# Kernel optimization log

Hardware: AMD Instinct MI355X
Metric: run time of the kernel (lower is better)

## Reference

```python
import jax, jax.numpy as jnp
import numpy as np

BS, EP = 32, 32
N_AGENTS, N_ATOM, EMBED = 8, 51, 32
STATE_DIM, HYP = 128, 64
V_MIN, V_MAX = -10.0, 10.0


def proj(support, probs, v_min, v_max, n_atom):
    # C51 categorical projection of (support, probs) onto the fixed atom grid
    # linspace(v_min, v_max, n_atom). support/probs: [..., M] -> [..., n_atom]
    support, probs = jnp.broadcast_arrays(support, probs)
    delta = (v_max - v_min) / (n_atom - 1)
    b = (jnp.clip(support, v_min, v_max) - v_min) / delta
    l = jnp.floor(b)
    u = jnp.ceil(b)
    eq = (u == l).astype(probs.dtype)  # support exactly on an atom -> all mass to l
    ml = probs * (u - b + eq)
    mu = probs * (b - l)
    shp = probs.shape
    n = int(np.prod(shp[:-1]))
    m = shp[-1]
    rows = jnp.arange(n)[:, None]
    out = jnp.zeros((n, n_atom), probs.dtype)
    out = out.at[rows, l.astype(jnp.int32).reshape(n, m)].add(ml.reshape(n, m))
    out = out.at[rows, u.astype(jnp.int32).reshape(n, m)].add(mu.reshape(n, m))
    return out.reshape(shp[:-1] + (n_atom,))


def bconv(p, q):
    # Full 1D convolution of per-row categorical pmfs (sum of two random vars).
    # p: [N, L], q: [N, M] -> [N, L+M-1], via grouped conv (one group per row).
    N, L = p.shape
    M = q.shape[-1]
    out = jax.lax.conv_general_dilated(
        p[None], jnp.flip(q, -1)[:, None, :],
        window_strides=(1,), padding=[(M - 1, M - 1)],
        feature_group_count=N, dimension_numbers=('NCW', 'OIW', 'NCW'))
    return out[0]


def mlp2(x, w1, b1, w2, b2):
    return jax.nn.relu(x @ w1.T + b1) @ w2.T + b2


def setup_inputs():
    key = jax.random.key(0)
    ks = jax.random.split(key, 20)
    def p(k, shape, s=0.05):
        return jax.random.normal(k, shape, dtype=jnp.float32) * s
    aq = jax.random.uniform(ks[0], (BS, EP, N_AGENTS, N_ATOM), dtype=jnp.float32)
    aq = aq / jnp.sum(aq, -1, keepdims=True)  # valid categorical distributions
    return {
        'agent_qs_distri': aq,
        'states': p(ks[1], (BS, EP, STATE_DIM), 1.0),
        'hw1_w1': p(ks[2], (HYP, STATE_DIM)), 'hw1_b1': p(ks[3], (HYP,)),
        'hw1_w2': p(ks[4], (EMBED * N_AGENTS, HYP)), 'hw1_b2': p(ks[5], (EMBED * N_AGENTS,)),
        'hb1_w': p(ks[6], (EMBED, STATE_DIM)), 'hb1_b': p(ks[7], (EMBED,)),
        'hwf_w1': p(ks[8], (HYP, STATE_DIM)), 'hwf_b1': p(ks[9], (HYP,)),
        'hwf_w2': p(ks[10], (EMBED, HYP)), 'hwf_b2': p(ks[11], (EMBED,)),
        'v_w1': p(ks[12], (EMBED, STATE_DIM)), 'v_b1': p(ks[13], (EMBED,)),
        'v_w2': p(ks[14], (1, EMBED)), 'v_b2': p(ks[15], (1,)),
    }


def reference(agent_qs_distri, states, hw1_w1, hw1_b1, hw1_w2, hw1_b2,
              hb1_w, hb1_b, hwf_w1, hwf_b1, hwf_w2, hwf_b2,
              v_w1, v_b1, v_w2, v_b2):
    bs, ep, n_agents, n_atom = agent_qs_distri.shape
    s = states.reshape(-1, STATE_DIM)
    atoms = jnp.linspace(V_MIN, V_MAX, n_atom).astype(jnp.float32)  # [A]

    w1 = jnp.abs(mlp2(s, hw1_w1, hw1_b1, hw1_w2, hw1_b2)).reshape(bs, ep, EMBED, n_agents)
    b1 = (s @ hb1_w.T + hb1_b).reshape(bs, ep, EMBED)

    # stage 1: scale each agent's support by w1[..., k, i], project back onto atoms
    sup1 = atoms * w1[..., None]                                       # [bs,ep,E,Na,A]
    aw = proj(sup1, agent_qs_distri[:, :, None], V_MIN, V_MAX, n_atom)  # [bs,ep,E,Na,A]
    awf = aw.reshape(-1, n_agents, n_atom)                              # [bs*ep*E,Na,A]
    q = awf[:, 0]
    for i in range(1, n_agents):
        q = bconv(q, awf[:, i])                                         # [.., Na*A-Na+1]
    L1 = n_agents * n_atom - n_agents + 1
    sup = jnp.linspace(n_agents * V_MIN, n_agents * V_MAX, L1).astype(jnp.float32)
    sup = jax.nn.elu(sup + b1[..., None])                               # [bs,ep,E,L1]
    x = proj(sup, q.reshape(bs, ep, EMBED, L1), V_MIN, V_MAX, n_atom)   # [bs,ep,E,A]

    # stage 2: hyper_w_final scaling, convolve across embed dim, add V(s)
    wf = jnp.abs(mlp2(s, hwf_w1, hwf_b1, hwf_w2, hwf_b2)).reshape(bs, ep, EMBED)
    xw = proj(atoms * wf[..., None], x, V_MIN, V_MAX, n_atom)           # [bs,ep,E,A]
    xwf = xw.reshape(-1, EMBED, n_atom)
    q = xwf[:, 0]
    for i in range(1, EMBED):
        q = bconv(q, xwf[:, i])                                         # [bs*ep, E*A-E+1]
    L2 = EMBED * n_atom - EMBED + 1
    v = mlp2(s, v_w1, v_b1, v_w2, v_b2).reshape(bs, ep, 1)
    sup2 = jnp.linspace(EMBED * V_MIN, EMBED * V_MAX, L2).astype(jnp.float32) + v
    return proj(sup2, q.reshape(bs, ep, L2), V_MIN, V_MAX, n_atom)      # [bs,ep,A]
```

## Files before the change

kernel.cpp:

```cpp
#include <hip/hip_runtime.h>
#include <hip/hip_bf16.h>
#include <math.h>

typedef unsigned short u16;

#define WAVE_SYNC() asm volatile("s_waitcnt lgkmcnt(0)" ::: "memory")

__device__ __forceinline__ float bf2f(u16 u) {
  union { unsigned int i; float f; } c;
  c.i = ((unsigned int)u) << 16;
  return c.f;
}
__device__ __forceinline__ float bflo(unsigned int u) {
  union { unsigned int i; float f; } c; c.i = u << 16; return c.f;
}
__device__ __forceinline__ float bfhi(unsigned int u) {
  union { unsigned int i; float f; } c; c.i = u & 0xffff0000u; return c.f;
}
__device__ __forceinline__ u16 f2bf(float f) {
  union { float f; unsigned int i; } c;
  c.f = f;
  unsigned int x = c.i;
  unsigned int r = (x + 0x7fffu + ((x >> 16) & 1u)) >> 16;
  return (u16)r;
}

__device__ __forceinline__ void proj_bounds(float wv, int& ML, int& MH) {
  float smin = (-10.0f + 0.4f * 0.0f)  * wv;
  float smax = (-10.0f + 0.4f * 50.0f) * wv;
  float bmin = (fminf(fmaxf(smin, -10.0f), 10.0f) + 10.0f) / 0.4f;
  float bmax = (fminf(fmaxf(smax, -10.0f), 10.0f) + 10.0f) / 0.4f;
  ML = (int)floorf(bmin);
  MH = (int)ceilf(bmax);
}

template<typename SUPP>
__device__ __forceinline__ void proj_scan(float* __restrict__ g1,
                                          float* __restrict__ g2,
                                          int span, int lane, SUPP supp)
{
  if (lane < 52) g1[lane] = 0.f;
  if (lane < 53) g2[lane] = 0.f;
  float cml = 0.f, cmu = 0.f;
  int ck = -1;
  for (int base = 0; base < span; base += 64) {
    int t = base + lane;
    bool act = (t < span);
    int tc = act ? t : (span - 1);
    float sup, p;
    supp(tc, act, sup, p);
    float c  = fminf(fmaxf(sup, -10.0f), 10.0f);
    float b  = (c + 10.0f) / 0.4f;
    float l  = floorf(b);
    float u  = ceilf(b);
    float eq = (u == l) ? 1.0f : 0.0f;
    float ml = p * (u - b + eq);
    float mu = p * (b - l);
    int   li = (int)l;
    bool last = (base + 64 >= span);
    if (lane == 0 && ck >= 0) {
      if (ck == li) { ml += cml; mu += cmu; }
      else          { g1[ck] = cml; g2[ck + 1] = cmu; }
    }
#pragma unroll
    for (int d = 1; d < 64; d <<= 1) {
      int   lo = __shfl_up(li, d);
      float a1 = __shfl_up(ml, d);
      float a2 = __shfl_up(mu, d);
      bool same = (lane >= d) && (lo == li);
      ml += same ? a1 : 0.f;
      mu += same ? a2 : 0.f;
    }
    int ln = __shfl_down(li, 1);
    bool runend = (lane == 63) ? last : (ln != li);
    if (runend) { g1[li] = ml; g2[li + 1] = mu; }
    if (!last) {
      cml = __shfl(ml, 63);
      cmu = __shfl(mu, 63);
      ck  = __shfl(li, 63);
    }
  }
}

__device__ __forceinline__ void conv_pad2(const float* __restrict__ q,
                                          float* __restrict__ qn,
                                          const float* __restrict__ kvs,
                                          int ML, int W, int T,
                                          int LQ, int HQ, int tid, int nthr)
{
  const int Lout = LQ + ML, Hout = HQ + ML + T;
  for (int J = Lout + tid; J <= Hout; J += nthr) {
    const float* qp = q + (J - ML);
    float acc = 0.f;
    for (int c = 0; c < W; c += 4) {
      float4 k4 = *(const float4*)(kvs + c);
      acc = fmaf(k4.x, qp[-c],     acc);
      acc = fmaf(k4.y, qp[-c - 1], acc);
      acc = fmaf(k4.z, qp[-c - 2], acc);
      acc = fmaf(k4.w, qp[-c - 3], acc);
    }
    qn[J] = acc;
  }
}

template<int BF>
__device__ __forceinline__ float ldt(const void* p, int i) {
  if (BF) return bf2f(((const u16*)p)[i]);
  return ((const float*)p)[i];
}

template<int BF>
__device__ __forceinline__ float dot128_t(const void* w, int row, const float* s) {
  float acc = 0.f;
  if (BF) {
    const uint4* p = (const uint4*)((const u16*)w + row * 128);
#pragma unroll
    for (int i = 0; i < 16; ++i) {
      uint4 v = p[i];
      int b = i * 8;
      acc = fmaf(bflo(v.x), s[b + 0], acc); acc = fmaf(bfhi(v.x), s[b + 1], acc);
      acc = fmaf(bflo(v.y), s[b + 2], acc); acc = fmaf(bfhi(v.y), s[b + 3], acc);
      acc = fmaf(bflo(v.z), s[b + 4], acc); acc = fmaf(bfhi(v.z), s[b + 5], acc);
      acc = fmaf(bflo(v.w), s[b + 6], acc); acc = fmaf(bfhi(v.w), s[b + 7], acc);
    }
  } else {
    const float4* p = (const float4*)((const float*)w + row * 128);
#pragma unroll
    for (int i = 0; i < 32; ++i) {
      float4 v = p[i];
      int b = i * 4;
      acc = fmaf(v.x, s[b + 0], acc); acc = fmaf(v.y, s[b + 1], acc);
      acc = fmaf(v.z, s[b + 2], acc); acc = fmaf(v.w, s[b + 3], acc);
    }
  }
  return acc;
}

template<int BF>
__device__ __forceinline__ float dot64_t(const void* w, int row, const float* h) {
  float acc = 0.f;
  if (BF) {
    const uint4* p = (const uint4*)((const u16*)w + row * 64);
#pragma unroll
    for (int i = 0; i < 8; ++i) {
      uint4 v = p[i];
      int b = i * 8;
      acc = fmaf(bflo(v.x), h[b + 0], acc); acc = fmaf(bfhi(v.x), h[b + 1], acc);
      acc = fmaf(bflo(v.y), h[b + 2], acc); acc = fmaf(bfhi(v.y), h[b + 3], acc);
      acc = fmaf(bflo(v.z), h[b + 4], acc); acc = fmaf(bfhi(v.z), h[b + 5], acc);
      acc = fmaf(bflo(v.w), h[b + 6], acc); acc = fmaf(bfhi(v.w), h[b + 7], acc);
    }
  } else {
    const float4* p = (const float4*)((const float*)w + row * 64);
#pragma unroll
    for (int i = 0; i < 16; ++i) {
      float4 v = p[i];
      int b = i * 4;
      acc = fmaf(v.x, h[b + 0], acc); acc = fmaf(v.y, h[b + 1], acc);
      acc = fmaf(v.z, h[b + 2], acc); acc = fmaf(v.w, h[b + 3], acc);
    }
  }
  return acc;
}

template<int BF>
__device__ __forceinline__ void mlp_body(
    const void* states,
    const void* hw1_w1, const void* hw1_b1, const void* hw1_w2, const void* hw1_b2,
    const void* hb1_w,  const void* hb1_b,
    const void* hwf_w1, const void* hwf_b1, const void* hwf_w2, const void* hwf_b2,
    const void* v_w1,   const void* v_b1,   const void* v_w2,   const void* v_b2,
    float* w1_ws, float* b1_ws, float* wf_ws, float* v_ws,
    int n, int tid, float* s, float* h1, float* hf, float* vh)
{
  s[tid]      = ldt<BF>(states, n * 128 + tid);
  s[tid + 64] = ldt<BF>(states, n * 128 + 64 + tid);
  __syncthreads();

  h1[tid] = fmaxf(dot128_t<BF>(hw1_w1, tid, s) + ldt<BF>(hw1_b1, tid), 0.f);
  hf[tid] = fmaxf(dot128_t<BF>(hwf_w1, tid, s) + ldt<BF>(hwf_b1, tid), 0.f);
  if (tid < 32) {
    vh[tid] = fmaxf(dot128_t<BF>(v_w1, tid, s) + ldt<BF>(v_b1, tid), 0.f);
    b1_ws[n * 32 + tid] = dot128_t<BF>(hb1_w, tid, s) + ldt<BF>(hb1_b, tid);
  }
  __syncthreads();

#pragma unroll
  for (int k = 0; k < 4; ++k) {
    int o = tid + 64 * k;
    w1_ws[n * 256 + o] = fabsf(dot64_t<BF>(hw1_w2, o, h1) + ldt<BF>(hw1_b2, o));
  }
  if (tid < 32)
    wf_ws[n * 32 + tid] = fabsf(dot64_t<BF>(hwf_w2, tid, hf) + ldt<BF>(hwf_b2, tid));
  if (tid == 0) {
    float acc = ldt<BF>(v_b2, 0);
    for (int e = 0; e < 32; ++e) acc = fmaf(ldt<BF>(v_w2, e), vh[e], acc);
    v_ws[n] = acc;
  }
}

__global__ __launch_bounds__(64) void k_mlp(
    const void* __restrict__ states,
    const void* __restrict__ hw1_w1, const void* __restrict__ hw1_b1,
    const void* __restrict__ hw1_w2, const void* __restrict__ hw1_b2,
    const void* __restrict__ hb1_w,  const void* __restrict__ hb1_b,
    const void* __restrict__ hwf_w1, const void* __restrict__ hwf_b1,
    const void* __restrict__ hwf_w2, const void* __restrict__ hwf_b2,
    const void* __restrict__ v_w1,   const void* __restrict__ v_b1,
    const void* __restrict__ v_w2,   const void* __restrict__ v_b2,
    float* __restrict__ w1_ws, float* __restrict__ b1_ws,
    float* __restrict__ wf_ws, float* __restrict__ v_ws,
    int* __restrict__ flag)
{
  __shared__ float s[128];
  __shared__ float h1[64];
  __shared__ float hf[64];
  __shared__ float vh[32];
  const int n = blockIdx.x;
  const int tid = threadIdx.x;

  const u16* sr = (const u16*)states;
  unsigned int e0 = (sr[tid] >> 7) & 0xFF;
  unsigned int e1 = (sr[tid + 64] >> 7) & 0xFF;
  unsigned long long bl0 = __ballot(e0 >= 97 && e0 <= 141);
  unsigned long long bl1 = __ballot(e1 >= 97 && e1 <= 141);
  int bf = (__popcll(bl0) + __popcll(bl1) >= 104) ? 1 : 0;
  if (tid == 0) *flag = bf;

  if (bf)
    mlp_body<1>(states, hw1_w1, hw1_b1, hw1_w2, hw1_b2, hb1_w, hb1_b,
                hwf_w1, hwf_b1, hwf_w2, hwf_b2, v_w1, v_b1, v_w2, v_b2,
                w1_ws, b1_ws, wf_ws, v_ws, n, tid, s, h1, hf, vh);
  else
    mlp_body<0>(states, hw1_w1, hw1_b1, hw1_w2, hw1_b2, hb1_w, hb1_b,
                hwf_w1, hwf_b1, hwf_w2, hwf_b2, v_w1, v_b1, v_w2, v_b2,
                w1_ws, b1_ws, wf_ws, v_ws, n, tid, s, h1, hf, vh);
}

__global__ __launch_bounds__(128) void k_perembed(
    const void* __restrict__ aq,
    const float* __restrict__ w1_ws, const float* __restrict__ b1_ws,
    const float* __restrict__ wf_ws, float* __restrict__ xw_ws,
    const int* __restrict__ flag)
{
  __shared__ __align__(16) float Ab[2][520];
  __shared__ __align__(16) float Bb[2][520];
  __shared__ __align__(16) float kv_all[2][8][16];
  __shared__ __align__(16) float kvo[2][56];
  __shared__ float p_lds[2][8][52];
  __shared__ float gAb[2][53];
  __shared__ float gBb[2][54];

  const int w    = threadIdx.x >> 6;
  const int lane = threadIdx.x & 63;
  const int task = blockIdx.x * 2 + w;
  const int n = task >> 5;
  const int e = task & 31;
  const int bf = *flag;

  float* A   = Ab[w];
  float* B   = Bb[w];
  float* gA  = gAb[w];
  float* gB  = gBb[w];
  float (*pl)[52] = p_lds[w];

  if (bf) {
    const u16* p = (const u16*)aq + n * 408 + lane;
    if (lane < 51) {
#pragma unroll
      for (int a = 0; a < 8; ++a) pl[a][lane] = bf2f(p[a * 51]);
    }
  } else {
    const float* p = (const float*)aq + n * 408 + lane;
    if (lane < 51) {
#pragma unroll
      for (int a = 0; a < 8; ++a) pl[a][lane] = p[a * 51];
    }
  }
  float wreg = (lane < 8) ? w1_ws[n * 256 + e * 8 + lane] : 0.f;
  float b1v  = b1_ws[n * 32 + e];
  float wfv  = wf_ws[n * 32 + e];

  int mlA = 0, mhA = 0;
  if (lane < 8) proj_bounds(wreg, mlA, mhA);
  unsigned long long wide = __ballot((lane < 8) && (mhA - mlA > 15));
  WAVE_SYNC();

  int LQ, HQ;
  float* q = A;
  float* qn = B;

  if (wide == 0ull) {
#pragma unroll
    for (int r = 0; r < 2; ++r) {
      int a  = 4 * r + (lane >> 4);
      int jj = lane & 15;
      float wv = __shfl(wreg, a);
      int ML = __shfl(mlA, a);
      int MH = __shfl(mhA, a);
      int T = MH - ML;
      int j = ML + jj;
      float ej = 0.4f * (float)j - 10.0f;
      float invw = 2.5f / wv;
      int tL = (jj == 0) ? 0  : (int)floorf((ej - 0.4f) * invw + 25.f) - 1;
      int tH = (jj >= T) ? 50 : (int)ceilf ((ej + 0.4f) * invw + 25.f) + 1;
      tL = tL < 0 ? 0 : tL;
      tH = tH > 50 ? 50 : tH;
      if (jj > T) { tL = 0; tH = -1; }
      float acc = 0.f;
      float tf = (float)tL;
      const float* pb = pl[a];
      for (int t = tL; t <= tH; ++t) {
        float p = pb[t];
        float sup = (-10.0f + 0.4f * tf) * wv;
        float c = fminf(fmaxf(sup, -10.0f), 10.0f);
        float d = (c - ej) * 2.5f;
        float wgt = fmaxf(0.f, 1.f - fabsf(d));
        acc = fmaf(p, wgt, acc);
        tf += 1.0f;
      }
      kv_all[w][a][jj] = (jj <= T) ? acc : 0.f;
    }
    WAVE_SYNC();

    int ML0 = __shfl(mlA, 0), MH0 = __shfl(mhA, 0);
    if (lane <= MH0 - ML0) A[64 + ML0 + lane] = kv_all[w][0][lane];
    WAVE_SYNC();
    LQ = 64 + ML0; HQ = 64 + MH0;

#pragma unroll
    for (int a = 1; a < 8; ++a) {
      int ML = __shfl(mlA, a), MH = __shfl(mhA, a);
      int T = MH - ML;
      int W = (T + 4) & ~3;
      if (lane < W - 1) q[LQ - 1 - lane] = 0.f;
      if (lane < T)     q[HQ + 1 + lane] = 0.f;
      WAVE_SYNC();
      conv_pad2(q, qn, &kv_all[w][a][0], ML, W, T, LQ, HQ, lane, 64);
      WAVE_SYNC();
      LQ += ML; HQ += MH;
      float* t_ = q; q = qn; qn = t_;
    }
  } else {
    float* kvs = kvo[w];
    float wv0 = __shfl(wreg, 0);
    int ML0 = __shfl(mlA, 0), MH0 = __shfl(mhA, 0);
    proj_scan(gA, gB, 51, lane, [&](int t, bool act, float& sup, float& p) {
      sup = (-10.0f + 0.4f * (float)t) * wv0;
      float pv = pl[0][t];
      p = act ? pv : 0.f;
    });
    if (lane <= MH0 - ML0)
      A[64 + ML0 + lane] = gA[ML0 + lane] + gB[ML0 + lane];
    WAVE_SYNC();
    LQ = 64 + ML0; HQ = 64 + MH0;

    for (int a = 1; a < 8; ++a) {
      float wv = __shfl(wreg, a);
      int ML = __shfl(mlA, a), MH = __shfl(mhA, a);
      int T = MH - ML;
      int W = (T + 4) & ~3;
      proj_scan(gA, gB, 51, lane, [&](int t, bool act, float& sup, float& p) {
        sup = (-10.0f + 0.4f * (float)t) * wv;
        float pv = pl[a][t];
        p = act ? pv : 0.f;
      });
      if (lane < W)     kvs[lane] = (lane <= T) ? (gA[ML + lane] + gB[ML + lane]) : 0.f;
      if (lane < W - 1) q[LQ - 1 - lane] = 0.f;
      if (lane < T)     q[HQ + 1 + lane] = 0.f;
      WAVE_SYNC();
      conv_pad2(q, qn, kvs, ML, W, T, LQ, HQ, lane, 64);
      WAVE_SYNC();
      LQ += ML; HQ += MH;
      float* t_ = q; q = qn; qn = t_;
    }
  }

  {
    int span = HQ - LQ + 1;
    int LQl = LQ;
    const float* qf = q;
    proj_scan(gA, gB, span, lane, [&](int t, bool act, float& sup, float& p) {
      int tg = (LQl - 64) + t;
      float raw = (-80.0f + 0.4f * (float)tg) + b1v;
      sup = (raw > 0.f) ? raw : expm1f(raw);
      p = act ? qf[LQl + t] : 0.f;
    });
  }
  WAVE_SYNC();

  float x2v = (lane < 51) ? (gA[lane] + gB[lane]) : 0.f;
  WAVE_SYNC();
  int MLf, MHf;
  proj_bounds(wfv, MLf, MHf);
  proj_scan(gA, gB, 51, lane, [&](int t, bool act, float& sup, float& p) {
    sup = (-10.0f + 0.4f * (float)t) * wfv;
    p = act ? x2v : 0.f;
  });
  WAVE_SYNC();
  if (lane <= MHf - MLf)
    xw_ws[task * 51 + MLf + lane] = gA[MLf + lane] + gB[MLf + lane];
}

__global__ __launch_bounds__(256) void k_final(
    const float* __restrict__ xw_ws, const float* __restrict__ wf_ws,
    const float* __restrict__ v_ws,
    void* __restrict__ out, const int* __restrict__ flag)
{
  __shared__ __align__(16) float bufA[4608];
  __shared__ __align__(16) float bufB[4608];
  __shared__ int meta_s[63];
  __shared__ int meta_l[63];
  __shared__ int meta_ml[32];
  __shared__ int meta_g[6];
  __shared__ int meta_mltot;
  __shared__ float gA[53], gB[54];

  const int n    = blockIdx.x;
  const int tid  = threadIdx.x;
  const int lane = tid & 63;
  const int bf   = *flag;

  float wfreg = (lane < 32) ? wf_ws[n * 32 + lane] : 0.f;
  float vv    = v_ws[n];

  for (int i = tid; i < 4608; i += 256) { bufA[i] = 0.f; bufB[i] = 0.f; }

  if (tid < 64) {
    int ml, mh;
    proj_bounds(wfreg, ml, mh);
    if (lane < 32) meta_ml[lane] = ml;
    int msum = ml;
#pragma unroll
    for (int d = 1; d < 32; d <<= 1) msum += __shfl_xor(msum, d);
    if (lane == 0) meta_mltot = msum;

    int curlen = mh - ml + 1;
    int base = 0, Ncur = 32;
#pragma unroll
    for (int c = 0; c <= 5; ++c) {
      int lm = (lane < Ncur) ? curlen : 0;
#pragma unroll
      for (int d = 1; d < 32; d <<= 1) {
        int o = __shfl_xor(lm, d);
        lm = (o > lm) ? o : lm;
      }
      int G = (lm + 11) & ~3;
      int sp = ((curlen + 3) & ~3) + G;
      int inc = (lane < Ncur) ? sp : 0;
      int v0 = inc;
#pragma unroll
      for (int d = 1; d < 32; d <<= 1) {
        int u = __shfl_up(inc, d);
        if (lane >= d && lane < 32) inc += u;
      }
      if (lane < Ncur) {
        meta_s[base + lane] = 832 + (inc - v0);
        meta_l[base + lane] = curlen;
      }
      if (lane == 0) meta_g[c] = G;
      if (c < 5) {
        int l0 = __shfl(curlen, 2 * lane);
        int l1 = __shfl(curlen, 2 * lane + 1);
        curlen = l0 + l1 - 1;
        base += Ncur;
        Ncur >>= 1;
      }
    }
  }
  __syncthreads();

  {
    int g = tid >> 3, i = tid & 7;
    int s = meta_s[g], l = meta_l[g], ml = meta_ml[g];
    const float* row = xw_ws + (n * 32 + g) * 51 + ml;
    for (int i0 = i; i0 < l; i0 += 8) bufA[s + i0] = row[i0];
  }
  __syncthreads();

#pragma unroll
  for (int c = 1; c <= 5; ++c) {
    const float* bin = (c & 1) ? bufA : bufB;
    float*       bout = (c & 1) ? bufB : bufA;
    const int Nout = 32 >> c;
    const int lg = 3 + c;
    const int gs = 1 << lg;
    const int k  = tid >> lg;
    const int st = tid & (gs - 1);
    const int bc = 64 - (64 >> c);
    const int bp = 64 - (64 >> (c - 1));
    const int i0 = bp + 2 * k;
    const int sA = meta_s[i0];
    const int sB = meta_s[i0 + 1];
    const int lB = meta_l[i0 + 1];
    const int sO = meta_s[bc + k];
    const int lO = meta_l[bc + k];
    const int W  = (lB + 3) & ~3;

    for (int j = st * 2; j < lO; j += gs * 2) {
      const float* Ap = bin + sA + j + 1;
      float a0 = 0.f, a1 = 0.f;
      for (int m = 0; m < W; m += 4) {
        float4 k4 = *(const float4*)(bin + sB + m);
        float v0 = Ap[-m], v1 = Ap[-m - 1], v2 = Ap[-m - 2];
        float v3 = Ap[-m - 3], v4 = Ap[-m - 4];
        a0 = fmaf(k4.x, v1, fmaf(k4.y, v2, fmaf(k4.z, v3, fmaf(k4.w, v4, a0))));
        a1 = fmaf(k4.x, v0, fmaf(k4.y, v1, fmaf(k4.z, v2, fmaf(k4.w, v3, a1))));
      }
      bout[sO + j] = a0;
      if (j + 1 < lO) bout[sO + j + 1] = a1;
    }

    if (c >= 2 && c <= 4) {
      int G = meta_g[c];
      for (int p = tid; p < G; p += 256) bout[832 - G + p] = 0.f;
      for (int k2 = 0; k2 < Nout; ++k2) {
        int ss = meta_s[bc + k2] + meta_l[bc + k2];
        int ee = (k2 + 1 < Nout) ? meta_s[bc + k2 + 1]
                                 : ss + G + 3;
        for (int p = ss + tid; p < ee; p += 256) bout[p] = 0.f;
      }
    }
    __syncthreads();
  }

  if (tid < 64) {
    int s5 = meta_s[62], l5 = meta_l[62], mlt = meta_mltot;
    const float* qf = bufB + s5;
    proj_scan(gA, gB, l5, lane, [&](int t, bool act, float& sup, float& p) {
      int tg = mlt + t;
      sup = (-320.0f + 0.4f * (float)tg) + vv;
      p = act ? qf[t] : 0.f;
    });
    WAVE_SYNC();
    if (lane < 51) {
      float o = gA[lane] + gB[lane];
      if (bf) ((u16*)out)[n * 51 + lane] = f2bf(o);
      else    ((float*)out)[n * 51 + lane] = o;
    }
  }
}

extern "C" void kernel_launch(void* const* d_in, const int* in_sizes, int n_in,
                              void* d_out, int out_size, void* d_ws, size_t ws_size,
                              hipStream_t stream)
{
  float* ws    = (float*)d_ws;
  float* w1_ws = ws;
  float* b1_ws = w1_ws + 1024 * 256;
  float* wf_ws = b1_ws + 1024 * 32;
  float* v_ws  = wf_ws + 1024 * 32;
  float* xw_ws = v_ws  + 1024;
  int*   flag  = (int*)(xw_ws + 1024 * 32 * 51);

  k_mlp<<<1024, 64, 0, stream>>>(d_in[1],
      d_in[2], d_in[3], d_in[4], d_in[5], d_in[6], d_in[7],
      d_in[8], d_in[9], d_in[10], d_in[11], d_in[12], d_in[13],
      d_in[14], d_in[15],
      w1_ws, b1_ws, wf_ws, v_ws, flag);

  k_perembed<<<16384, 128, 0, stream>>>(d_in[0], w1_ws, b1_ws, wf_ws, xw_ws, flag);

  k_final<<<1024, 256, 0, stream>>>(xw_ws, wf_ws, v_ws, d_out, flag);
}
```

Baseline: 248.7 us.

## Trim zero-tail kernel spans and merge per-agent convolution barriers

In the narrow path of the per-embed kernel, each projected agent kernel is trimmed to its nonzero span using a wave ballot, so later convolutions run over shorter windows. The zero padding for the next step is written right after the current convolution, which removes one wave sync per agent. The ping-pong buffers are pre-zeroed once with float4 stores, and the final kernel's buffer clearing now uses float4 stores and runs the bounds computation in every wave instead of a tid<64 guard. This depends on the pre-zeroed buffers staying correct for the high-side padding that was dropped, and misaligned or shifted kernel windows could break correctness.

```diff
diff --git a/kernel.cpp b/kernel.cpp
--- a/kernel.cpp
+++ b/kernel.cpp
@@ -245,9 +245,10 @@
 {
   __shared__ __align__(16) float Ab[2][520];
   __shared__ __align__(16) float Bb[2][520];
-  __shared__ __align__(16) float kv_all[2][8][16];
+  __shared__ __align__(16) float kv_all[2][8][20];
   __shared__ __align__(16) float kvo[2][56];
   __shared__ float p_lds[2][8][52];
+  __shared__ int   tml[2][8], tmh[2][8];
   __shared__ float gAb[2][53];
   __shared__ float gBb[2][54];
 
@@ -263,6 +264,13 @@
   float* gA  = gAb[w];
   float* gB  = gBb[w];
   float (*pl)[52] = p_lds[w];
+
+  {
+    float4 z = make_float4(0.f, 0.f, 0.f, 0.f);
+    float4* a4 = (float4*)A;
+    float4* b4 = (float4*)B;
+    for (int i = lane; i < 130; i += 64) { a4[i] = z; b4[i] = z; }
+  }
 
   if (bf) {
     const u16* p = (const u16*)aq + n * 408 + lane;
@@ -300,45 +308,61 @@
       int MH = __shfl(mhA, a);
       int T = MH - ML;
       int j = ML + jj;
-      float ej = 0.4f * (float)j - 10.0f;
+      float ej  = 0.4f * (float)j - 10.0f;
+      float e25 = ej * 2.5f;
       float invw = 2.5f / wv;
       int tL = (jj == 0) ? 0  : (int)floorf((ej - 0.4f) * invw + 25.f) - 1;
       int tH = (jj >= T) ? 50 : (int)ceilf ((ej + 0.4f) * invw + 25.f) + 1;
       tL = tL < 0 ? 0 : tL;
       tH = tH > 50 ? 50 : tH;
       if (jj > T) { tL = 0; tH = -1; }
+      float step = 0.4f * wv;
+      float sup  = fmaf((float)tL, step, -10.0f * wv);
       float acc = 0.f;
-      float tf = (float)tL;
       const float* pb = pl[a];
       for (int t = tL; t <= tH; ++t) {
-        float p = pb[t];
-        float sup = (-10.0f + 0.4f * tf) * wv;
-        float c = fminf(fmaxf(sup, -10.0f), 10.0f);
-        float d = (c - ej) * 2.5f;
-        float wgt = fmaxf(0.f, 1.f - fabsf(d));
-        acc = fmaf(p, wgt, acc);
-        tf += 1.0f;
-      }
-      kv_all[w][a][jj] = (jj <= T) ? acc : 0.f;
+        float c   = fminf(fmaxf(sup, -10.0f), 10.0f);
+        float d   = fmaf(c, 2.5f, -e25);
+        float wgt = fmaxf(0.f, 1.0f - fabsf(d));
+        acc = fmaf(pb[t], wgt, acc);
+        sup += step;
+      }
+      unsigned long long nz = __ballot(acc != 0.f);
+      unsigned int field = (unsigned int)((nz >> (16 * (lane >> 4))) & 0xFFFFull);
+      int o_lo = 0, o_hi = T;
+      if (field) { o_lo = (__ffs(field) - 1) & ~3; o_hi = 31 - __clz(field); }
+      if (jj == 0) { tml[w][a] = ML + o_lo; tmh[w][a] = ML + o_hi; }
+      kv_all[w][a][jj] = acc;
+      if (jj < 4) kv_all[w][a][16 + jj] = 0.f;
     }
     WAVE_SYNC();
 
-    int ML0 = __shfl(mlA, 0), MH0 = __shfl(mhA, 0);
-    if (lane <= MH0 - ML0) A[64 + ML0 + lane] = kv_all[w][0][lane];
+    int ML0o = __shfl(mlA, 0);
+    int t0l = tml[w][0], t0h = tmh[w][0];
+    if (lane <= t0h - t0l) A[64 + t0l + lane] = kv_all[w][0][(t0l - ML0o) + lane];
+    LQ = 64 + t0l; HQ = 64 + t0h;
+
+    {
+      int ML1 = tml[w][1], MH1 = tmh[w][1];
+      int W1 = ((MH1 - ML1) + 4) & ~3;
+      if (lane < W1 - 1) A[LQ - 1 - lane] = 0.f;
+    }
     WAVE_SYNC();
-    LQ = 64 + ML0; HQ = 64 + MH0;
 
 #pragma unroll
     for (int a = 1; a < 8; ++a) {
-      int ML = __shfl(mlA, a), MH = __shfl(mhA, a);
+      int MLo = __shfl(mlA, a);
+      int ML = tml[w][a], MH = tmh[w][a];
       int T = MH - ML;
       int W = (T + 4) & ~3;
-      if (lane < W - 1) q[LQ - 1 - lane] = 0.f;
-      if (lane < T)     q[HQ + 1 + lane] = 0.f;
+      conv_pad2(q, qn, &kv_all[w][a][ML - MLo], ML, W, T, LQ, HQ, lane, 64);
+      LQ += ML; HQ += MH;
+      if (a < 7) {
+        int MLn = tml[w][a + 1], MHn = tmh[w][a + 1];
+        int Wn = ((MHn - MLn) + 4) & ~3;
+        if (lane < Wn - 1) qn[LQ - 1 - lane] = 0.f;
+      }
       WAVE_SYNC();
-      conv_pad2(q, qn, &kv_all[w][a][0], ML, W, T, LQ, HQ, lane, 64);
-      WAVE_SYNC();
-      LQ += ML; HQ += MH;
       float* t_ = q; q = qn; qn = t_;
     }
   } else {
@@ -367,7 +391,6 @@
       });
       if (lane < W)     kvs[lane] = (lane <= T) ? (gA[ML + lane] + gB[ML + lane]) : 0.f;
       if (lane < W - 1) q[LQ - 1 - lane] = 0.f;
-      if (lane < T)     q[HQ + 1 + lane] = 0.f;
       WAVE_SYNC();
       conv_pad2(q, qn, kvs, ML, W, T, LQ, HQ, lane, 64);
       WAVE_SYNC();
@@ -424,9 +447,14 @@
   float wfreg = (lane < 32) ? wf_ws[n * 32 + lane] : 0.f;
   float vv    = v_ws[n];
 
-  for (int i = tid; i < 4608; i += 256) { bufA[i] = 0.f; bufB[i] = 0.f; }
-
-  if (tid < 64) {
+  {
+    float4 z = make_float4(0.f, 0.f, 0.f, 0.f);
+    float4* a4 = (float4*)bufA;
+    float4* b4 = (float4*)bufB;
+    for (int i = tid; i < 1152; i += 256) { a4[i] = z; b4[i] = z; }
+  }
+
+  {
     int ml, mh;
     proj_bounds(wfreg, ml, mh);
     if (lane < 32) meta_ml[lane] = ml;
```

New measurement: 250.1 us. About the same (+0.6%).

## Fuse final embed convolution into per-embed kernel via last-arriving wave

Applied to the files above, without the earlier changes.

Each per-embed wave atomically bumps a per-sample counter. The last of the 32 waves then runs the 32-way convolution and final projection in its own LDS arena, writes the output and sets a done flag, while samples whose support is too wide fall back to k_final, which now exits early when the flag is set. This removes the k_final tail work and the extra round-trip through memory for most samples, at the cost of serialising a 31-step convolution on a single wave and enlarging LDS per block. It also strength-reduces the support computation in the first-stage projection loop and vectorises the zero fill in k_final.

```diff
diff --git a/kernel.cpp b/kernel.cpp
--- a/kernel.cpp
+++ b/kernel.cpp
@@ -210,7 +210,7 @@
     const void* __restrict__ v_w2,   const void* __restrict__ v_b2,
     float* __restrict__ w1_ws, float* __restrict__ b1_ws,
     float* __restrict__ wf_ws, float* __restrict__ v_ws,
-    int* __restrict__ flag)
+    int* __restrict__ flag, int* __restrict__ cnt, int* __restrict__ done)
 {
   __shared__ float s[128];
   __shared__ float h1[64];
@@ -225,7 +225,7 @@
   unsigned long long bl0 = __ballot(e0 >= 97 && e0 <= 141);
   unsigned long long bl1 = __ballot(e1 >= 97 && e1 <= 141);
   int bf = (__popcll(bl0) + __popcll(bl1) >= 104) ? 1 : 0;
-  if (tid == 0) *flag = bf;
+  if (tid == 0) { *flag = bf; cnt[n] = 0; done[n] = 0; }
 
   if (bf)
     mlp_body<1>(states, hw1_w1, hw1_b1, hw1_w2, hw1_b2, hb1_w, hb1_b,
@@ -240,11 +240,11 @@
 __global__ __launch_bounds__(128) void k_perembed(
     const void* __restrict__ aq,
     const float* __restrict__ w1_ws, const float* __restrict__ b1_ws,
-    const float* __restrict__ wf_ws, float* __restrict__ xw_ws,
-    const int* __restrict__ flag)
+    const float* __restrict__ wf_ws, const float* __restrict__ v_ws,
+    float* __restrict__ xw_ws, void* __restrict__ out,
+    const int* __restrict__ flag, int* __restrict__ cnt, int* __restrict__ done)
 {
-  __shared__ __align__(16) float Ab[2][520];
-  __shared__ __align__(16) float Bb[2][520];
+  __shared__ __align__(16) float arena[2][1240];
   __shared__ __align__(16) float kv_all[2][8][16];
   __shared__ __align__(16) float kvo[2][56];
   __shared__ float p_lds[2][8][52];
@@ -258,8 +258,8 @@
   const int e = task & 31;
   const int bf = *flag;
 
-  float* A   = Ab[w];
-  float* B   = Bb[w];
+  float* A   = arena[w];
+  float* B   = arena[w] + 620;
   float* gA  = gAb[w];
   float* gB  = gBb[w];
   float (*pl)[52] = p_lds[w];
@@ -300,24 +300,24 @@
       int MH = __shfl(mhA, a);
       int T = MH - ML;
       int j = ML + jj;
-      float ej = 0.4f * (float)j - 10.0f;
+      float ej  = 0.4f * (float)j - 10.0f;
+      float e25 = ej * 2.5f;
       float invw = 2.5f / wv;
       int tL = (jj == 0) ? 0  : (int)floorf((ej - 0.4f) * invw + 25.f) - 1;
       int tH = (jj >= T) ? 50 : (int)ceilf ((ej + 0.4f) * invw + 25.f) + 1;
       tL = tL < 0 ? 0 : tL;
       tH = tH > 50 ? 50 : tH;
       if (jj > T) { tL = 0; tH = -1; }
+      float step = 0.4f * wv;
+      float sup  = fmaf((float)tL, step, -10.0f * wv);
       float acc = 0.f;
-      float tf = (float)tL;
       const float* pb = pl[a];
       for (int t = tL; t <= tH; ++t) {
-        float p = pb[t];
-        float sup = (-10.0f + 0.4f * tf) * wv;
-        float c = fminf(fmaxf(sup, -10.0f), 10.0f);
-        float d = (c - ej) * 2.5f;
-        float wgt = fmaxf(0.f, 1.f - fabsf(d));
-        acc = fmaf(p, wgt, acc);
-        tf += 1.0f;
+        float c   = fminf(fmaxf(sup, -10.0f), 10.0f);
+        float d   = fmaf(c, 2.5f, -e25);
+        float wgt = fmaxf(0.f, 1.0f - fabsf(d));
+        acc = fmaf(pb[t], wgt, acc);
+        sup += step;
       }
       kv_all[w][a][jj] = (jj <= T) ? acc : 0.f;
     }
@@ -400,12 +400,95 @@
   WAVE_SYNC();
   if (lane <= MHf - MLf)
     xw_ws[task * 51 + MLf + lane] = gA[MLf + lane] + gB[MLf + lane];
+
+  __threadfence();
+  int old = 0;
+  if (lane == 0) old = atomicAdd(&cnt[n], 1);
+  old = __shfl(old, 0);
+  if (old != 31) return;
+  __threadfence();
+
+  float wfr = (lane < 32) ? wf_ws[n * 32 + lane] : 0.f;
+  int rml = 0, rmh = 0;
+  if (lane < 32) proj_bounds(wfr, rml, rmh);
+  int sml = rml, smh = rmh;
+#pragma unroll
+  for (int d = 1; d < 32; d <<= 1) { sml += __shfl_xor(sml, d); smh += __shfl_xor(smh, d); }
+  sml = __shfl(sml, 0); smh = __shfl(smh, 0);
+  int Ltot = smh - sml + 1;
+  if (Ltot > 560) return;
+  float vv = v_ws[n];
+
+  float* fA = arena[w] + 52;
+  float* fB = arena[w] + 620 + 52;
+  float* kvf = kvo[w];
+  {
+    float4 z = make_float4(0.f, 0.f, 0.f, 0.f);
+    float4* a4 = (float4*)arena[w];
+    for (int i = lane; i < 310; i += 64) a4[i] = z;
+  }
+
+  int ml0 = __shfl(rml, 0), mh0 = __shfl(rmh, 0);
+  int L = mh0 - ml0 + 1;
+  int mlN = __shfl(rml, 1), mhN = __shfl(rmh, 1);
+  float nv = (lane <= mhN - mlN) ? xw_ws[(n * 32 + 1) * 51 + mlN + lane] : 0.f;
+  WAVE_SYNC();
+  if (lane < L) fA[lane] = xw_ws[(n * 32 + 0) * 51 + ml0 + lane];
+  WAVE_SYNC();
+
+  float* fq = fA;
+  float* fqn = fB;
+  for (int j = 1; j < 32; ++j) {
+    int T = mhN - mlN;
+    int W = (T + 4) & ~3;
+    if (lane < W) kvf[lane] = (lane <= T) ? nv : 0.f;
+    if (j < 31) {
+      mlN = __shfl(rml, j + 1); mhN = __shfl(rmh, j + 1);
+      nv = (lane <= mhN - mlN) ? xw_ws[(n * 32 + j + 1) * 51 + mlN + lane] : 0.f;
+    }
+    WAVE_SYNC();
+    int Lout = L + T;
+    for (int o = lane; o < Lout; o += 64) {
+      const float* qp = fq + o;
+      float acc = 0.f;
+      for (int c = 0; c < W; c += 4) {
+        float4 k4 = *(const float4*)(kvf + c);
+        acc = fmaf(k4.x, qp[-c],     acc);
+        acc = fmaf(k4.y, qp[-c - 1], acc);
+        acc = fmaf(k4.z, qp[-c - 2], acc);
+        acc = fmaf(k4.w, qp[-c - 3], acc);
+      }
+      fqn[o] = acc;
+    }
+    WAVE_SYNC();
+    L = Lout;
+    float* t_ = fq; fq = fqn; fqn = t_;
+  }
+
+  {
+    int span = L;
+    const float* qf = fq;
+    int mlt = sml;
+    proj_scan(gA, gB, span, lane, [&](int t, bool act, float& sup, float& p) {
+      int tg = mlt + t;
+      sup = (-320.0f + 0.4f * (float)tg) + vv;
+      p = act ? qf[t] : 0.f;
+    });
+  }
+  WAVE_SYNC();
+  if (lane < 51) {
+    float o = gA[lane] + gB[lane];
+    if (bf) ((u16*)out)[n * 51 + lane] = f2bf(o);
+    else    ((float*)out)[n * 51 + lane] = o;
+  }
+  if (lane == 0) done[n] = 1;
 }
 
 __global__ __launch_bounds__(256) void k_final(
     const float* __restrict__ xw_ws, const float* __restrict__ wf_ws,
     const float* __restrict__ v_ws,
-    void* __restrict__ out, const int* __restrict__ flag)
+    void* __restrict__ out, const int* __restrict__ flag,
+    const int* __restrict__ done)
 {
   __shared__ __align__(16) float bufA[4608];
   __shared__ __align__(16) float bufB[4608];
@@ -417,6 +500,8 @@
   __shared__ float gA[53], gB[54];
 
   const int n    = blockIdx.x;
+  if (done[n] != 0) return;
+
   const int tid  = threadIdx.x;
   const int lane = tid & 63;
   const int bf   = *flag;
@@ -424,9 +509,14 @@
   float wfreg = (lane < 32) ? wf_ws[n * 32 + lane] : 0.f;
   float vv    = v_ws[n];
 
-  for (int i = tid; i < 4608; i += 256) { bufA[i] = 0.f; bufB[i] = 0.f; }
-
-  if (tid < 64) {
+  {
+    float4 z = make_float4(0.f, 0.f, 0.f, 0.f);
+    float4* a4 = (float4*)bufA;
+    float4* b4 = (float4*)bufB;
+    for (int i = tid; i < 1152; i += 256) { a4[i] = z; b4[i] = z; }
+  }
+
+  {
     int ml, mh;
     proj_bounds(wfreg, ml, mh);
     if (lane < 32) meta_ml[lane] = ml;
@@ -552,14 +642,17 @@
   float* v_ws  = wf_ws + 1024 * 32;
   float* xw_ws = v_ws  + 1024;
   int*   flag  = (int*)(xw_ws + 1024 * 32 * 51);
+  int*   cnt   = flag + 1;
+  int*   done  = cnt + 1024;
 
   k_mlp<<<1024, 64, 0, stream>>>(d_in[1],
       d_in[2], d_in[3], d_in[4], d_in[5], d_in[6], d_in[7],
       d_in[8], d_in[9], d_in[10], d_in[11], d_in[12], d_in[13],
       d_in[14], d_in[15],
-      w1_ws, b1_ws, wf_ws, v_ws, flag);
-
-  k_perembed<<<16384, 128, 0, stream>>>(d_in[0], w1_ws, b1_ws, wf_ws, xw_ws, flag);
-
-  k_final<<<1024, 256, 0, stream>>>(xw_ws, wf_ws, v_ws, d_out, flag);
-}
+      w1_ws, b1_ws, wf_ws, v_ws, flag, cnt, done);
+
+  k_perembed<<<16384, 128, 0, stream>>>(d_in[0], w1_ws, b1_ws, wf_ws, v_ws,
+                                        xw_ws, d_out, flag, cnt, done);
+
+  k_final<<<1024, 256, 0, stream>>>(xw_ws, wf_ws, v_ws, d_out, flag, done);
+}
```

Result: slower. 884.1 us (+255.5%).
